# Performance work log

Measured on AMD Instinct MI355X. Metric: run time of the kernel, lower is better.

The kernel has to match this reference:

```python
import jax, jax.numpy as jnp
import numpy as np

KS = 3            # kernel_size per axis
K3 = KS * KS * KS  # 27 flattened kernel bins
_OFFSETS = np.array([[dz, dy, dx] for dz in (0, 1) for dy in (0, 1) for dx in (0, 1)], np.int32)  # 8 trilinear corners
_STRIDES = np.array([KS * KS, KS, 1], np.int32)
EPS = 1e-12


def continuous_conv(features, pos_input, pos_output, extents, kernel, bias):
    """Open3D-style ContinuousConv: ball_to_cube_radial mapping, poly6 window,
    trilinear kernel interpolation, per-output-point weighted aggregate."""
    No, Ni = pos_output.shape[0], pos_input.shape[0]
    # normalized relative positions: unit ball of radius extents/2 -> r in [0,1)
    rel = (pos_input[None, :, :] - pos_output[:, None, :]) * (2.0 / extents[0])  # [No,Ni,3]
    r2 = jnp.sum(rel * rel, axis=-1)                                             # [No,Ni]
    inside = r2 < 1.0
    window = jnp.where(inside, (1.0 - r2) ** 3, 0.0)        # poly6 window, zero outside support
    r = jnp.sqrt(jnp.maximum(r2, EPS))
    linf = jnp.max(jnp.abs(rel), axis=-1)
    # radial ball->cube map: scale each point by ||p||_2 / ||p||_inf
    scale = jnp.where(linf > EPS, r / jnp.maximum(linf, EPS), 1.0)
    q = jnp.clip(rel * scale[..., None], -1.0, 1.0)         # cube coords in [-1,1]^3
    t = (q + 1.0) * 0.5 * (KS - 1)                          # grid coords in [0, KS-1]
    t0 = jnp.clip(jnp.floor(t), 0, KS - 2).astype(jnp.int32)
    f = t - t0                                              # trilinear fractions [No,Ni,3]
    off = jnp.asarray(_OFFSETS)                             # [8,3]
    cw = jnp.where(off[None, None, :, :] == 1, f[:, :, None, :], 1.0 - f[:, :, None, :])
    w8 = cw.prod(axis=-1) * window[:, :, None]              # [No,Ni,8] corner weights
    idx8 = jnp.sum((t0[:, :, None, :] + off) * jnp.asarray(_STRIDES), axis=-1)  # [No,Ni,8] flat bin
    ii = jnp.arange(No)[:, None, None]
    jj = jnp.arange(Ni)[None, :, None]
    # A[i,j,k]: interpolation weight of input j into kernel bin k for output i
    A = jnp.zeros((No, Ni, K3), features.dtype).at[ii, jj, idx8].add(w8)
    B = jnp.einsum('ijk,jc->ikc', A, features)              # aggregate features per bin
    out = jnp.einsum('ikc,kcf->if', B, kernel) + bias       # contract with learned kernel
    return out


def setup_inputs() -> dict:
    key = jax.random.key(0)
    k1, k2, k3, k4 = jax.random.split(key, 4)
    N_IN, N_OUT, C_IN, C_OUT = 2048, 2048, 8, 64
    features = jax.random.normal(k1, (N_IN, C_IN), dtype=jnp.float32)
    pos_input = jax.random.uniform(k2, (N_IN, 3), dtype=jnp.float32)
    pos_output = jax.random.uniform(k3, (N_OUT, 3), dtype=jnp.float32)
    extents = jnp.ones((1,), dtype=jnp.float32)
    kernel = jax.random.normal(k4, (K3, C_IN, C_OUT), dtype=jnp.float32) * 0.05
    bias = jnp.zeros((C_OUT,), dtype=jnp.float32)
    return {"features": features, "pos_input": pos_input, "pos_output": pos_output,
            "extents": extents, "kernel": kernel, "bias": bias}


def reference(features, pos_input, pos_output, extents, kernel, bias):
    x = continuous_conv(features, pos_input, pos_output, extents, kernel, bias)
    return jax.nn.relu(x)
```

## Files before the change

kernel.cpp:

```cpp
#include <hip/hip_runtime.h>

#define K3 27
#define CIN 8
#define COUT 64
#define CC_EPS 1e-12f
#define NI_CAP 2048

__global__ __launch_bounds__(256)
void cconv_fused_kernel(const float* __restrict__ features,
                        const float* __restrict__ pos_input,
                        const float* __restrict__ pos_output,
                        const float* __restrict__ extents,
                        const float* __restrict__ kern,
                        const float* __restrict__ bias,
                        float* __restrict__ out,
                        int Ni, int No)
{
    const int tid  = threadIdx.x;
    const int w    = tid >> 6;
    const int lane = tid & 63;
    const int i    = blockIdx.x;

    __shared__ unsigned short idx[NI_CAP];
    __shared__ int   cnt_sh;
    __shared__ float Bsh[4][K3][CIN];
    __shared__ float Bf[K3][CIN];
    __shared__ float part[4][COUT];

    if (tid == 0) cnt_sh = 0;
    __syncthreads();

    const float s  = 2.0f / extents[0];
    const float ox = pos_output[i * 3 + 0];
    const float oy = pos_output[i * 3 + 1];
    const float oz = pos_output[i * 3 + 2];

    for (int j0 = w * 64; j0 < Ni; j0 += 256) {
        const int j = j0 + lane;
        bool inside = false;
        if (j < Ni) {
            const float rx = (pos_input[j * 3 + 0] - ox) * s;
            const float ry = (pos_input[j * 3 + 1] - oy) * s;
            const float rz = (pos_input[j * 3 + 2] - oz) * s;
            inside = (rx * rx + ry * ry + rz * rz) < 1.0f;
        }
        const unsigned long long m = __ballot(inside);
        const int nin = (int)__popcll(m);
        int base = 0;
        if (lane == 0 && nin) base = atomicAdd(&cnt_sh, nin);
        base = __shfl(base, 0, 64);
        if (inside) {
            const int pre = __popcll(m & ((1ull << lane) - 1ull));
            idx[base + pre] = (unsigned short)j;
        }
    }
    __syncthreads();
    const int total = cnt_sh;

    float acc[K3];
#pragma unroll
    for (int k = 0; k < K3; ++k) acc[k] = 0.0f;

    const int jsub = lane >> 3;
    const int c    = lane & 7;
    for (int base = w * 8; base < total; base += 32) {
        const int  slot  = base + jsub;
        const bool valid = (slot < total);
        const int  j     = idx[valid ? slot : total - 1];

        const float rx = (pos_input[j * 3 + 0] - ox) * s;
        const float ry = (pos_input[j * 3 + 1] - oy) * s;
        const float rz = (pos_input[j * 3 + 2] - oz) * s;
        const float fval = valid ? features[j * CIN + c] : 0.0f;

        const float r2  = rx * rx + ry * ry + rz * rz;
        const float u   = 1.0f - r2;
        const float win = u * u * u;
        const float r    = __builtin_amdgcn_sqrtf(fmaxf(r2, CC_EPS));
        const float linf = fmaxf(fmaxf(fabsf(rx), fabsf(ry)), fabsf(rz));
        const float scale = (linf > CC_EPS) ? r * __builtin_amdgcn_rcpf(linf) : 1.0f;
        const float ta = fminf(fmaxf(rx * scale, -1.f), 1.f) + 1.0f;
        const float tb = fminf(fmaxf(ry * scale, -1.f), 1.f) + 1.0f;
        const float tc = fminf(fmaxf(rz * scale, -1.f), 1.f) + 1.0f;
        const float wa0 = fmaxf(1.0f - ta, 0.0f), wa2 = fmaxf(ta - 1.0f, 0.0f);
        const float wb0 = fmaxf(1.0f - tb, 0.0f), wb2 = fmaxf(tb - 1.0f, 0.0f);
        const float wc0 = fmaxf(1.0f - tc, 0.0f), wc2 = fmaxf(tc - 1.0f, 0.0f);
        const float wa1 = 1.0f - wa0 - wa2;
        const float wb1 = 1.0f - wb0 - wb2;
        const float wc1 = 1.0f - wc0 - wc2;

        const float wav[3] = { wa0 * win,  wa1 * win,  wa2 * win  };
        const float wbv[3] = { wb0,        wb1,        wb2        };
        const float wcf[3] = { wc0 * fval, wc1 * fval, wc2 * fval };
#pragma unroll
        for (int a = 0; a < 3; ++a) {
#pragma unroll
            for (int b = 0; b < 3; ++b) {
                const float wab = wav[a] * wbv[b];
#pragma unroll
                for (int c3 = 0; c3 < 3; ++c3) {
                    acc[a * 9 + b * 3 + c3] =
                        fmaf(wab, wcf[c3], acc[a * 9 + b * 3 + c3]);
                }
            }
        }
    }

#pragma unroll
    for (int k = 0; k < K3; ++k) {
        float v = acc[k];
        v += __shfl_xor(v, 8, 64);
        v += __shfl_xor(v, 16, 64);
        v += __shfl_xor(v, 32, 64);
        acc[k] = v;
    }
    if (jsub == 0) {
#pragma unroll
        for (int k = 0; k < K3; ++k) Bsh[w][k][c] = acc[k];
    }
    __syncthreads();

    if (tid < K3 * CIN) {
        const int k  = tid >> 3;
        const int cc = tid & 7;
        Bf[k][cc] = Bsh[0][k][cc] + Bsh[1][k][cc] + Bsh[2][k][cc] + Bsh[3][k][cc];
    }
    __syncthreads();

    {
        const int kb = w * 7;
        const int ke = (kb + 7 < K3) ? kb + 7 : K3;
        const int f  = lane;
        float o = 0.0f;
        for (int k = kb; k < ke; ++k) {
#pragma unroll
            for (int cc = 0; cc < CIN; ++cc) {
                o = fmaf(Bf[k][cc], kern[(k * CIN + cc) * COUT + f], o);
            }
        }
        part[w][f] = o;
    }
    __syncthreads();

    if (tid < COUT) {
        const float o = bias[tid] + part[0][tid] + part[1][tid]
                                  + part[2][tid] + part[3][tid];
        out[i * COUT + tid] = fmaxf(o, 0.0f);
    }
}

extern "C" void kernel_launch(void* const* d_in, const int* in_sizes, int n_in,
                              void* d_out, int out_size, void* d_ws, size_t ws_size,
                              hipStream_t stream) {
    const float* features   = (const float*)d_in[0];
    const float* pos_input  = (const float*)d_in[1];
    const float* pos_output = (const float*)d_in[2];
    const float* extents    = (const float*)d_in[3];
    const float* kern       = (const float*)d_in[4];
    const float* bias       = (const float*)d_in[5];
    float* out = (float*)d_out;

    const int Ni = in_sizes[0] / CIN;
    const int No = in_sizes[2] / 3;

    dim3 block(256);
    dim3 grid(No);
    cconv_fused_kernel<<<grid, block, 0, stream>>>(features, pos_input, pos_output,
                                                   extents, kern, bias, out, Ni, No);
}
```

Before: 98.72 us.

## Compute per-neighbor trilinear weights once per point and share via LDS

The weight computation (sqrt, rcp, clamps, window) was previously repeated by all 8 channel lanes of each neighbor. Now 32 lanes per wave each compute one neighbor's 9 ab-products and 3 c-weights and write them to a per-wave LDS record. All lanes then read these records as float4s and do only the channel FMAs. Shared memory is overlapped via aliasing and launch bounds request 8 blocks for higher occupancy, at the cost of extra LDS traffic, a per-chunk wait, and half of each wave sitting idle during the weight phase.

```diff
diff --git a/kernel.cpp b/kernel.cpp
--- a/kernel.cpp
+++ b/kernel.cpp
@@ -4,9 +4,10 @@
 #define CIN 8
 #define COUT 64
 #define CC_EPS 1e-12f
-#define NI_CAP 2048
+#define CHUNK 32
+#define RECW 12
 
-__global__ __launch_bounds__(256)
+__global__ __launch_bounds__(256, 8)
 void cconv_fused_kernel(const float* __restrict__ features,
                         const float* __restrict__ pos_input,
                         const float* __restrict__ pos_output,
@@ -19,30 +20,33 @@
     const int tid  = threadIdx.x;
     const int w    = tid >> 6;
     const int lane = tid & 63;
+    const int g    = lane >> 3;
+    const int c    = lane & 7;
     const int i    = blockIdx.x;
 
-    __shared__ unsigned short idx[NI_CAP];
-    __shared__ int   cnt_sh;
-    __shared__ float Bsh[4][K3][CIN];
-    __shared__ float Bf[K3][CIN];
-    __shared__ float part[4][COUT];
+    __shared__ __align__(16) char smem[4096 + 4*CHUNK*RECW*4 + 4*K3*CIN*4];
+    unsigned short* idx  = (unsigned short*)smem;
+    float*          part = (float*)smem;
+    float*          wrec = (float*)(smem + 4096);
+    float*          Bsh  = (float*)(smem + 4096 + 4*CHUNK*RECW*4);
+    __shared__ int cnt_sh;
 
     if (tid == 0) cnt_sh = 0;
     __syncthreads();
 
     const float s  = 2.0f / extents[0];
-    const float ox = pos_output[i * 3 + 0];
-    const float oy = pos_output[i * 3 + 1];
-    const float oz = pos_output[i * 3 + 2];
+    const float ox = pos_output[i*3+0];
+    const float oy = pos_output[i*3+1];
+    const float oz = pos_output[i*3+2];
 
-    for (int j0 = w * 64; j0 < Ni; j0 += 256) {
+    for (int j0 = w*64; j0 < Ni; j0 += 256) {
         const int j = j0 + lane;
         bool inside = false;
         if (j < Ni) {
-            const float rx = (pos_input[j * 3 + 0] - ox) * s;
-            const float ry = (pos_input[j * 3 + 1] - oy) * s;
-            const float rz = (pos_input[j * 3 + 2] - oz) * s;
-            inside = (rx * rx + ry * ry + rz * rz) < 1.0f;
+            const float rx = (pos_input[j*3+0]-ox)*s;
+            const float ry = (pos_input[j*3+1]-oy)*s;
+            const float rz = (pos_input[j*3+2]-oz)*s;
+            inside = (rx*rx + ry*ry + rz*rz) < 1.0f;
         }
         const unsigned long long m = __ballot(inside);
         const int nin = (int)__popcll(m);
@@ -50,8 +54,8 @@
         if (lane == 0 && nin) base = atomicAdd(&cnt_sh, nin);
         base = __shfl(base, 0, 64);
         if (inside) {
-            const int pre = __popcll(m & ((1ull << lane) - 1ull));
-            idx[base + pre] = (unsigned short)j;
+            const int pre = __popcll(m & ((1ull<<lane)-1ull));
+            idx[base+pre] = (unsigned short)j;
         }
     }
     __syncthreads();
@@ -61,46 +65,63 @@
 #pragma unroll
     for (int k = 0; k < K3; ++k) acc[k] = 0.0f;
 
-    const int jsub = lane >> 3;
-    const int c    = lane & 7;
-    for (int base = w * 8; base < total; base += 32) {
-        const int  slot  = base + jsub;
-        const bool valid = (slot < total);
-        const int  j     = idx[valid ? slot : total - 1];
+    for (int cb = w*CHUNK; cb < total; cb += 4*CHUNK) {
+        if (lane < CHUNK) {
+            const int  slot = cb + lane;
+            const bool va   = slot < total;
+            const int  j    = idx[va ? slot : 0];
+            float ab0=0,ab1=0,ab2=0,ab3=0,ab4=0,ab5=0,ab6=0,ab7=0,ab8=0;
+            float wc0=0,wc1=0,wc2=0;
+            if (va) {
+                const float rx = (pos_input[j*3+0]-ox)*s;
+                const float ry = (pos_input[j*3+1]-oy)*s;
+                const float rz = (pos_input[j*3+2]-oz)*s;
+                const float r2  = rx*rx + ry*ry + rz*rz;
+                const float u   = 1.0f - r2;
+                const float win = u*u*u;
+                const float r    = __builtin_amdgcn_sqrtf(fmaxf(r2, CC_EPS));
+                const float linf = fmaxf(fmaxf(fabsf(rx), fabsf(ry)), fabsf(rz));
+                const float scale = (linf > CC_EPS) ? r*__builtin_amdgcn_rcpf(linf) : 1.0f;
+                const float ta = fminf(fmaxf(rx*scale, -1.f), 1.f) + 1.0f;
+                const float tb = fminf(fmaxf(ry*scale, -1.f), 1.f) + 1.0f;
+                const float tc = fminf(fmaxf(rz*scale, -1.f), 1.f) + 1.0f;
+                const float wa0 = fmaxf(1.0f-ta, 0.0f), wa2 = fmaxf(ta-1.0f, 0.0f);
+                const float wb0 = fmaxf(1.0f-tb, 0.0f), wb2 = fmaxf(tb-1.0f, 0.0f);
+                wc0 = fmaxf(1.0f-tc, 0.0f); wc2 = fmaxf(tc-1.0f, 0.0f);
+                const float wa1 = 1.0f - wa0 - wa2;
+                const float wb1 = 1.0f - wb0 - wb2;
+                wc1 = 1.0f - wc0 - wc2;
+                const float a0 = wa0*win, a1 = wa1*win, a2 = wa2*win;
+                ab0 = a0*wb0; ab1 = a0*wb1; ab2 = a0*wb2;
+                ab3 = a1*wb0; ab4 = a1*wb1; ab5 = a1*wb2;
+                ab6 = a2*wb0; ab7 = a2*wb1; ab8 = a2*wb2;
+            }
+            float* rec = wrec + (w*CHUNK + lane)*RECW;
+            ((float4*)rec)[0] = make_float4(ab0, ab1, ab2, ab3);
+            ((float4*)rec)[1] = make_float4(ab4, ab5, ab6, ab7);
+            ((float4*)rec)[2] = make_float4(ab8, wc0, wc1, wc2);
+        }
+        asm volatile("s_waitcnt lgkmcnt(0)" ::: "memory");
+        __builtin_amdgcn_sched_barrier(0);
 
-        const float rx = (pos_input[j * 3 + 0] - ox) * s;
-        const float ry = (pos_input[j * 3 + 1] - oy) * s;
-        const float rz = (pos_input[j * 3 + 2] - oz) * s;
-        const float fval = valid ? features[j * CIN + c] : 0.0f;
-
-        const float r2  = rx * rx + ry * ry + rz * rz;
-        const float u   = 1.0f - r2;
-        const float win = u * u * u;
-        const float r    = __builtin_amdgcn_sqrtf(fmaxf(r2, CC_EPS));
-        const float linf = fmaxf(fmaxf(fabsf(rx), fabsf(ry)), fabsf(rz));
-        const float scale = (linf > CC_EPS) ? r * __builtin_amdgcn_rcpf(linf) : 1.0f;
-        const float ta = fminf(fmaxf(rx * scale, -1.f), 1.f) + 1.0f;
-        const float tb = fminf(fmaxf(ry * scale, -1.f), 1.f) + 1.0f;
-        const float tc = fminf(fmaxf(rz * scale, -1.f), 1.f) + 1.0f;
-        const float wa0 = fmaxf(1.0f - ta, 0.0f), wa2 = fmaxf(ta - 1.0f, 0.0f);
-        const float wb0 = fmaxf(1.0f - tb, 0.0f), wb2 = fmaxf(tb - 1.0f, 0.0f);
-        const float wc0 = fmaxf(1.0f - tc, 0.0f), wc2 = fmaxf(tc - 1.0f, 0.0f);
-        const float wa1 = 1.0f - wa0 - wa2;
-        const float wb1 = 1.0f - wb0 - wb2;
-        const float wc1 = 1.0f - wc0 - wc2;
-
-        const float wav[3] = { wa0 * win,  wa1 * win,  wa2 * win  };
-        const float wbv[3] = { wb0,        wb1,        wb2        };
-        const float wcf[3] = { wc0 * fval, wc1 * fval, wc2 * fval };
 #pragma unroll
-        for (int a = 0; a < 3; ++a) {
+        for (int t = 0; t < CHUNK/8; ++t) {
+            const int l    = t*8 + g;
+            const int slot = cb + l;
+            const float* rec = wrec + (w*CHUNK + l)*RECW;
+            const float4 r0 = ((const float4*)rec)[0];
+            const float4 r1 = ((const float4*)rec)[1];
+            const float4 r2 = ((const float4*)rec)[2];
+            const int   jj = idx[slot < total ? slot : 0];
+            const float fv = features[jj*CIN + c];
+            const float wabv[9] = { r0.x, r0.y, r0.z, r0.w,
+                                    r1.x, r1.y, r1.z, r1.w, r2.x };
+            const float fcs[3]  = { r2.y*fv, r2.z*fv, r2.w*fv };
 #pragma unroll
-            for (int b = 0; b < 3; ++b) {
-                const float wab = wav[a] * wbv[b];
+            for (int ab = 0; ab < 9; ++ab) {
 #pragma unroll
-                for (int c3 = 0; c3 < 3; ++c3) {
-                    acc[a * 9 + b * 3 + c3] =
-                        fmaf(wab, wcf[c3], acc[a * 9 + b * 3 + c3]);
+                for (int cc = 0; cc < 3; ++cc) {
+                    acc[ab*3 + cc] = fmaf(wabv[ab], fcs[cc], acc[ab*3 + cc]);
                 }
             }
         }
@@ -114,38 +135,40 @@
         v += __shfl_xor(v, 32, 64);
         acc[k] = v;
     }
-    if (jsub == 0) {
+    if (g == 0) {
 #pragma unroll
-        for (int k = 0; k < K3; ++k) Bsh[w][k][c] = acc[k];
+        for (int k = 0; k < K3; ++k) Bsh[(w*K3 + k)*CIN + c] = acc[k];
     }
     __syncthreads();
 
-    if (tid < K3 * CIN) {
+    if (tid < K3*CIN) {
         const int k  = tid >> 3;
         const int cc = tid & 7;
-        Bf[k][cc] = Bsh[0][k][cc] + Bsh[1][k][cc] + Bsh[2][k][cc] + Bsh[3][k][cc];
+        Bsh[k*CIN + cc] = Bsh[k*CIN + cc]
+                        + Bsh[(K3   + k)*CIN + cc]
+                        + Bsh[(2*K3 + k)*CIN + cc]
+                        + Bsh[(3*K3 + k)*CIN + cc];
     }
     __syncthreads();
 
     {
-        const int kb = w * 7;
+        const int kb = w*7;
         const int ke = (kb + 7 < K3) ? kb + 7 : K3;
-        const int f  = lane;
         float o = 0.0f;
         for (int k = kb; k < ke; ++k) {
 #pragma unroll
             for (int cc = 0; cc < CIN; ++cc) {
-                o = fmaf(Bf[k][cc], kern[(k * CIN + cc) * COUT + f], o);
+                o = fmaf(Bsh[k*CIN + cc], kern[(k*CIN + cc)*COUT + lane], o);
             }
         }
-        part[w][f] = o;
+        part[w*COUT + lane] = o;
     }
     __syncthreads();
 
     if (tid < COUT) {
-        const float o = bias[tid] + part[0][tid] + part[1][tid]
-                                  + part[2][tid] + part[3][tid];
-        out[i * COUT + tid] = fmaxf(o, 0.0f);
+        const float o = bias[tid] + part[tid] + part[COUT + tid]
+                      + part[2*COUT + tid] + part[3*COUT + tid];
+        out[i*COUT + tid] = fmaxf(o, 0.0f);
     }
 }
 
```

Result: faster. 95.20 us (-3.6%).
